# Performance work log

Measured on AMD Instinct MI355X. Metric: run time of the kernel, lower is better.

## Reference

```python
import jax, jax.numpy as jnp
import numpy as np


def setup_inputs() -> dict:
    key = jax.random.key(0)
    kq, kk, kv = jax.random.split(key, 3)
    shape = (2, 8, 1024, 64)  # [B, H, L, D]
    return {
        "q": jax.random.normal(kq, shape, dtype=jnp.float32),
        "k": jax.random.normal(kk, shape, dtype=jnp.float32),
        "v": jax.random.normal(kv, shape, dtype=jnp.float32),
    }


def reference(q, k, v):
    B, H, L, D = q.shape
    eps = 1e-6
    q = jax.nn.relu(q).reshape(B * H, L, D)
    k = jax.nn.relu(k).reshape(B * H, L, D)
    v = jax.nn.relu(v).reshape(B * H, L, D)

    # cosFormer positional reweighting: pi/2 * (i+1)/L
    idx = (jnp.pi / 2) * jnp.arange(1, L + 1, dtype=q.dtype) / L  # [L]
    s = jnp.sin(idx)[None, :, None]  # [1, L, 1]
    c = jnp.cos(idx)[None, :, None]

    q_ = jnp.concatenate([q * s, q * c], axis=-1)  # [N, L, 2D]
    k_ = jnp.concatenate([k * s, k * c], axis=-1)  # [N, L, 2D]

    # causal linear attention via cumulative kv outer product
    kv = jnp.einsum("nld,nlm->nldm", k_, v)        # [N, L, 2D, D]
    kv_cum = jnp.cumsum(kv, axis=1)                  # [N, L, 2D, D]
    qkv = jnp.einsum("nld,nldm->nlm", q_, kv_cum)  # [N, L, D]

    k_cum = jnp.cumsum(k_, axis=1)                   # [N, L, 2D]
    denom = jnp.clip(jnp.einsum("nld,nld->nl", q_, k_cum), eps, None)

    out = qkv / denom[..., None]
    return out.reshape(B, H, L, D)
```

## Files before the change

### kernel.cpp

```cpp
#include <hip/hip_runtime.h>

#define N_HEADS 16
#define L_SEQ   1024
#define D_HEAD  64
#define D2      128
#define T_CHUNK 32
#define N_CHUNK (L_SEQ / T_CHUNK)
#define KV_ELEMS (D2 * D_HEAD)

#define ROWP 140
#define PARTP 132

__device__ __forceinline__ int pad_col(int d2) { return d2 + 4 * (d2 >> 5); }

#define SINCOS_SCALE 1.53398078788564122971e-3f

__device__ __forceinline__ float red8_dpp(float x) {
    x += __int_as_float(__builtin_amdgcn_mov_dpp(__float_as_int(x), 0xB1, 0xF, 0xF, true));
    x += __int_as_float(__builtin_amdgcn_mov_dpp(__float_as_int(x), 0x4E, 0xF, 0xF, true));
    x += __int_as_float(__builtin_amdgcn_mov_dpp(__float_as_int(x), 0x141, 0xF, 0xF, true));
    return x;
}
__device__ __forceinline__ float red16_dpp(float x) {
    x += __int_as_float(__builtin_amdgcn_mov_dpp(__float_as_int(x), 0xB1, 0xF, 0xF, true));
    x += __int_as_float(__builtin_amdgcn_mov_dpp(__float_as_int(x), 0x4E, 0xF, 0xF, true));
    x += __int_as_float(__builtin_amdgcn_mov_dpp(__float_as_int(x), 0x141, 0xF, 0xF, true));
    x += __int_as_float(__builtin_amdgcn_mov_dpp(__float_as_int(x), 0x140, 0xF, 0xF, true));
    return x;
}

__global__ __launch_bounds__(256, 2) void k1_chunk_sums(
    const float* __restrict__ k, const float* __restrict__ v,
    float* __restrict__ sumkv, float* __restrict__ sumk)
{
    __shared__ __attribute__((aligned(16))) float k_s[T_CHUNK][ROWP];
    __shared__ __attribute__((aligned(16))) float v_s[T_CHUNK][D_HEAD];
    __shared__ float s_tab[T_CHUNK], c_tab[T_CHUNK];

    const int c = blockIdx.x, n = blockIdx.y;
    const int tid = threadIdx.x;
    const int base = (n * L_SEQ + c * T_CHUNK) * D_HEAD;

    if (tid < T_CHUNK) {
        float th = SINCOS_SCALE * (float)(c * T_CHUNK + tid + 1);
        s_tab[tid] = __sinf(th);
        c_tab[tid] = __cosf(th);
    }
    __syncthreads();

    const float4* k4g = (const float4*)(k + base);
    const float4* v4g = (const float4*)(v + base);
#pragma unroll
    for (int j = 0; j < 2; ++j) {
        int i4 = j * 256 + tid;
        int l = i4 >> 4, d = (i4 & 15) << 2;
        float4 kk = k4g[i4], vv = v4g[i4];
        kk.x = fmaxf(kk.x, 0.f); kk.y = fmaxf(kk.y, 0.f);
        kk.z = fmaxf(kk.z, 0.f); kk.w = fmaxf(kk.w, 0.f);
        vv.x = fmaxf(vv.x, 0.f); vv.y = fmaxf(vv.y, 0.f);
        vv.z = fmaxf(vv.z, 0.f); vv.w = fmaxf(vv.w, 0.f);
        float s = s_tab[l], cs = c_tab[l];
        *(float4*)&k_s[l][pad_col(d)]      = make_float4(kk.x*s,  kk.y*s,  kk.z*s,  kk.w*s);
        *(float4*)&k_s[l][pad_col(d + 64)] = make_float4(kk.x*cs, kk.y*cs, kk.z*cs, kk.w*cs);
        *(float4*)&v_s[l][d] = vv;
    }
    __syncthreads();

    if (tid < D2) {
        int pc = pad_col(tid);
        float ks = 0.f;
#pragma unroll
        for (int l = 0; l < T_CHUNK; ++l) ks += k_s[l][pc];
        sumk[(n * N_CHUNK + c) * D2 + tid] = ks;
    }

    const int g = tid & 15, mb = (tid >> 4) << 2;
    const int gbase = pad_col(8 * g);

    float st[8][4];
#pragma unroll
    for (int i = 0; i < 8; ++i)
#pragma unroll
        for (int j = 0; j < 4; ++j) st[i][j] = 0.f;

    for (int l = 0; l < T_CHUNK; ++l) {
        float4 vv = *(const float4*)&v_s[l][mb];
        const float4* kf4 = (const float4*)&k_s[l][gbase];
        float4 ka = kf4[0], kb = kf4[1];
        float kf[8] = {ka.x, ka.y, ka.z, ka.w, kb.x, kb.y, kb.z, kb.w};
#pragma unroll
        for (int i = 0; i < 8; ++i) {
            st[i][0] = fmaf(kf[i], vv.x, st[i][0]);
            st[i][1] = fmaf(kf[i], vv.y, st[i][1]);
            st[i][2] = fmaf(kf[i], vv.z, st[i][2]);
            st[i][3] = fmaf(kf[i], vv.w, st[i][3]);
        }
    }

    float4* dst = (float4*)(sumkv + (size_t)(n * N_CHUNK + c) * KV_ELEMS);
#pragma unroll
    for (int i = 0; i < 8; ++i)
        dst[i * 256 + tid] = make_float4(st[i][0], st[i][1], st[i][2], st[i][3]);
}

__global__ __launch_bounds__(256) void k2_prefix(
    float* __restrict__ sumkv, float* __restrict__ sumk)
{
    const int x = blockIdx.x, n = blockIdx.y;
    const int tid = threadIdx.x;

    if (x < 32) {
        float* base = sumkv + (size_t)n * N_CHUNK * KV_ELEMS + x * 256 + tid;
        float t[N_CHUNK];
#pragma unroll
        for (int c = 0; c < N_CHUNK; ++c) t[c] = base[c * KV_ELEMS];
        float r = 0.f;
#pragma unroll
        for (int c = 0; c < N_CHUNK; ++c) { base[c * KV_ELEMS] = r; r += t[c]; }
    } else if (tid < D2) {
        float* bk = sumk + n * N_CHUNK * D2 + tid;
        float t[N_CHUNK];
#pragma unroll
        for (int c = 0; c < N_CHUNK; ++c) t[c] = bk[c * D2];
        float r = 0.f;
#pragma unroll
        for (int c = 0; c < N_CHUNK; ++c) { bk[c * D2] = r; r += t[c]; }
    }
}

__global__ __launch_bounds__(256, 2) void k3_output(
    const float* __restrict__ q, const float* __restrict__ k,
    const float* __restrict__ v, const float* __restrict__ sumkv,
    const float* __restrict__ sumk, float* __restrict__ out)
{
    __shared__ __attribute__((aligned(16))) float k_s[T_CHUNK][ROWP];
    __shared__ __attribute__((aligned(16))) float q_s[T_CHUNK][ROWP];
    __shared__ __attribute__((aligned(16))) float v_s[T_CHUNK][D_HEAD];
    __shared__ __attribute__((aligned(16))) float pool[T_CHUNK * PARTP];
    __shared__ float rden_s[T_CHUNK];
    __shared__ float s_tab[T_CHUNK], c_tab[T_CHUNK];

    float (*part_s)[PARTP] = (float(*)[PARTP])pool;
    float (*out_s)[D_HEAD] = (float(*)[D_HEAD])pool;

    const int c = blockIdx.x, n = blockIdx.y;
    const int tid = threadIdx.x;
    const int base = (n * L_SEQ + c * T_CHUNK) * D_HEAD;

    if (tid < T_CHUNK) {
        float th = SINCOS_SCALE * (float)(c * T_CHUNK + tid + 1);
        s_tab[tid] = __sinf(th);
        c_tab[tid] = __cosf(th);
    }
    __syncthreads();

    const float4* q4g = (const float4*)(q + base);
    const float4* k4g = (const float4*)(k + base);
    const float4* v4g = (const float4*)(v + base);
#pragma unroll
    for (int j = 0; j < 2; ++j) {
        int i4 = j * 256 + tid;
        int l = i4 >> 4, d = (i4 & 15) << 2;
        float4 kk = k4g[i4], qq = q4g[i4], vv = v4g[i4];
        kk.x = fmaxf(kk.x, 0.f); kk.y = fmaxf(kk.y, 0.f);
        kk.z = fmaxf(kk.z, 0.f); kk.w = fmaxf(kk.w, 0.f);
        qq.x = fmaxf(qq.x, 0.f); qq.y = fmaxf(qq.y, 0.f);
        qq.z = fmaxf(qq.z, 0.f); qq.w = fmaxf(qq.w, 0.f);
        vv.x = fmaxf(vv.x, 0.f); vv.y = fmaxf(vv.y, 0.f);
        vv.z = fmaxf(vv.z, 0.f); vv.w = fmaxf(vv.w, 0.f);
        float s = s_tab[l], cs = c_tab[l];
        *(float4*)&k_s[l][pad_col(d)]      = make_float4(kk.x*s,  kk.y*s,  kk.z*s,  kk.w*s);
        *(float4*)&k_s[l][pad_col(d + 64)] = make_float4(kk.x*cs, kk.y*cs, kk.z*cs, kk.w*cs);
        *(float4*)&q_s[l][pad_col(d)]      = make_float4(qq.x*s,  qq.y*s,  qq.z*s,  qq.w*s);
        *(float4*)&q_s[l][pad_col(d + 64)] = make_float4(qq.x*cs, qq.y*cs, qq.z*cs, qq.w*cs);
        *(float4*)&v_s[l][d] = vv;
    }

    const float4* pkv = (const float4*)(sumkv + (size_t)(n * N_CHUNK + c) * KV_ELEMS);
    float st[8][4];
#pragma unroll
    for (int i = 0; i < 8; ++i) {
        float4 p = pkv[i * 256 + tid];
        st[i][0] = p.x; st[i][1] = p.y; st[i][2] = p.z; st[i][3] = p.w;
    }
    float kc = 0.f;
    if (tid < D2) kc = sumk[(n * N_CHUNK + c) * D2 + tid];

    __syncthreads();

    if (tid < D2) {
        int pc = pad_col(tid);
#pragma unroll
        for (int l = 0; l < T_CHUNK; ++l) {
            kc += k_s[l][pc];
            part_s[l][tid] = q_s[l][pc] * kc;
        }
    }
    __syncthreads();

    {
        int l = tid >> 3, j = tid & 7;
        const float4* p4 = (const float4*)&part_s[l][j * 16];
        float4 aa = p4[0], bb = p4[1], cc = p4[2], dd = p4[3];
        float sum = ((aa.x + aa.y) + (aa.z + aa.w)) + ((bb.x + bb.y) + (bb.z + bb.w))
                  + ((cc.x + cc.y) + (cc.z + cc.w)) + ((dd.x + dd.y) + (dd.z + dd.w));
        sum = red8_dpp(sum);
        if (j == 0) rden_s[l] = 1.f / fmaxf(sum, 1e-6f);
    }
    __syncthreads();

    const int g = tid & 15, mb = (tid >> 4) << 2;
    const int gbase = pad_col(8 * g);

    for (int l = 0; l < T_CHUNK; ++l) {
        float4 vv = *(const float4*)&v_s[l][mb];
        const float4* kf4 = (const float4*)&k_s[l][gbase];
        const float4* qf4 = (const float4*)&q_s[l][gbase];
        float4 ka = kf4[0], kb = kf4[1];
        float4 qa = qf4[0], qb = qf4[1];
        float kf[8] = {ka.x, ka.y, ka.z, ka.w, kb.x, kb.y, kb.z, kb.w};
        float qf[8] = {qa.x, qa.y, qa.z, qa.w, qb.x, qb.y, qb.z, qb.w};
        float a0 = 0.f, a1 = 0.f, a2 = 0.f, a3 = 0.f;
#pragma unroll
        for (int i = 0; i < 8; ++i) {
            st[i][0] = fmaf(kf[i], vv.x, st[i][0]); a0 = fmaf(qf[i], st[i][0], a0);
            st[i][1] = fmaf(kf[i], vv.y, st[i][1]); a1 = fmaf(qf[i], st[i][1], a1);
            st[i][2] = fmaf(kf[i], vv.z, st[i][2]); a2 = fmaf(qf[i], st[i][2], a2);
            st[i][3] = fmaf(kf[i], vv.w, st[i][3]); a3 = fmaf(qf[i], st[i][3], a3);
        }
        a0 = red16_dpp(a0);
        a1 = red16_dpp(a1);
        a2 = red16_dpp(a2);
        a3 = red16_dpp(a3);
        if (g == 0) {
            float r = rden_s[l];
            *(float4*)&out_s[l][mb] = make_float4(a0 * r, a1 * r, a2 * r, a3 * r);
        }
    }
    __syncthreads();

    {
        float4* o4 = (float4*)(out + base);
        const float4* s4o = (const float4*)&out_s[0][0];
        o4[tid] = s4o[tid];
        o4[256 + tid] = s4o[256 + tid];
    }
}

extern "C" void kernel_launch(void* const* d_in, const int* in_sizes, int n_in,
                              void* d_out, int out_size, void* d_ws, size_t ws_size,
                              hipStream_t stream) {
    (void)in_sizes; (void)n_in; (void)out_size; (void)ws_size;
    const float* q = (const float*)d_in[0];
    const float* k = (const float*)d_in[1];
    const float* v = (const float*)d_in[2];
    float* out = (float*)d_out;

    float* sumkv = (float*)d_ws;
    float* sumk  = sumkv + (size_t)N_HEADS * N_CHUNK * KV_ELEMS;

    dim3 grid(N_CHUNK, N_HEADS);
    k1_chunk_sums<<<grid, 256, 0, stream>>>(k, v, sumkv, sumk);
    dim3 grid2(33, N_HEADS);
    k2_prefix<<<grid2, 256, 0, stream>>>(sumkv, sumk);
    k3_output<<<grid, 256, 0, stream>>>(q, k, v, sumkv, sumk, out);
}
```

Before: 92.55 us.

## Double threads per chunk block and vectorize prefix scan with float4

Block size for the chunk-sum and output kernels goes from 256 to 512 threads. Each thread now holds a 8x2 slice of the kv state instead of 8x4, which halves per-thread registers and serial FMA work and should raise occupancy and parallelism. The prefix kernel now scans float4 elements in two 16-chunk halves with 9 blocks per head instead of 33. The state layout in the workspace changes to match, and the denominator reduction switches to 16-lane DPP. The risk is more LDS reads per useful FMA and fewer, heavier blocks in the scan kernel.

```diff
diff --git a/kernel.cpp b/kernel.cpp
--- a/kernel.cpp
+++ b/kernel.cpp
@@ -15,12 +15,6 @@
 
 #define SINCOS_SCALE 1.53398078788564122971e-3f
 
-__device__ __forceinline__ float red8_dpp(float x) {
-    x += __int_as_float(__builtin_amdgcn_mov_dpp(__float_as_int(x), 0xB1, 0xF, 0xF, true));
-    x += __int_as_float(__builtin_amdgcn_mov_dpp(__float_as_int(x), 0x4E, 0xF, 0xF, true));
-    x += __int_as_float(__builtin_amdgcn_mov_dpp(__float_as_int(x), 0x141, 0xF, 0xF, true));
-    return x;
-}
 __device__ __forceinline__ float red16_dpp(float x) {
     x += __int_as_float(__builtin_amdgcn_mov_dpp(__float_as_int(x), 0xB1, 0xF, 0xF, true));
     x += __int_as_float(__builtin_amdgcn_mov_dpp(__float_as_int(x), 0x4E, 0xF, 0xF, true));
@@ -29,7 +23,7 @@
     return x;
 }
 
-__global__ __launch_bounds__(256, 2) void k1_chunk_sums(
+__global__ __launch_bounds__(512, 4) void k1_chunk_sums(
     const float* __restrict__ k, const float* __restrict__ v,
     float* __restrict__ sumkv, float* __restrict__ sumk)
 {
@@ -48,13 +42,11 @@
     }
     __syncthreads();
 
-    const float4* k4g = (const float4*)(k + base);
-    const float4* v4g = (const float4*)(v + base);
-#pragma unroll
-    for (int j = 0; j < 2; ++j) {
-        int i4 = j * 256 + tid;
-        int l = i4 >> 4, d = (i4 & 15) << 2;
-        float4 kk = k4g[i4], vv = v4g[i4];
+    {
+        const float4* k4g = (const float4*)(k + base);
+        const float4* v4g = (const float4*)(v + base);
+        int l = tid >> 4, d = (tid & 15) << 2;
+        float4 kk = k4g[tid], vv = v4g[tid];
         kk.x = fmaxf(kk.x, 0.f); kk.y = fmaxf(kk.y, 0.f);
         kk.z = fmaxf(kk.z, 0.f); kk.w = fmaxf(kk.w, 0.f);
         vv.x = fmaxf(vv.x, 0.f); vv.y = fmaxf(vv.y, 0.f);
@@ -74,33 +66,30 @@
         sumk[(n * N_CHUNK + c) * D2 + tid] = ks;
     }
 
-    const int g = tid & 15, mb = (tid >> 4) << 2;
+    const int g = tid & 15, mh = (tid >> 4) << 1;
     const int gbase = pad_col(8 * g);
 
-    float st[8][4];
-#pragma unroll
-    for (int i = 0; i < 8; ++i)
-#pragma unroll
-        for (int j = 0; j < 4; ++j) st[i][j] = 0.f;
+    float st0[8], st1[8];
+#pragma unroll
+    for (int j = 0; j < 8; ++j) { st0[j] = 0.f; st1[j] = 0.f; }
 
     for (int l = 0; l < T_CHUNK; ++l) {
-        float4 vv = *(const float4*)&v_s[l][mb];
+        float2 vm = *(const float2*)&v_s[l][mh];
         const float4* kf4 = (const float4*)&k_s[l][gbase];
         float4 ka = kf4[0], kb = kf4[1];
         float kf[8] = {ka.x, ka.y, ka.z, ka.w, kb.x, kb.y, kb.z, kb.w};
 #pragma unroll
         for (int i = 0; i < 8; ++i) {
-            st[i][0] = fmaf(kf[i], vv.x, st[i][0]);
-            st[i][1] = fmaf(kf[i], vv.y, st[i][1]);
-            st[i][2] = fmaf(kf[i], vv.z, st[i][2]);
-            st[i][3] = fmaf(kf[i], vv.w, st[i][3]);
+            st0[i] = fmaf(kf[i], vm.x, st0[i]);
+            st1[i] = fmaf(kf[i], vm.y, st1[i]);
         }
     }
 
     float4* dst = (float4*)(sumkv + (size_t)(n * N_CHUNK + c) * KV_ELEMS);
-#pragma unroll
-    for (int i = 0; i < 8; ++i)
-        dst[i * 256 + tid] = make_float4(st[i][0], st[i][1], st[i][2], st[i][3]);
+    dst[0 * 512 + tid] = make_float4(st0[0], st0[1], st0[2], st0[3]);
+    dst[1 * 512 + tid] = make_float4(st0[4], st0[5], st0[6], st0[7]);
+    dst[2 * 512 + tid] = make_float4(st1[0], st1[1], st1[2], st1[3]);
+    dst[3 * 512 + tid] = make_float4(st1[4], st1[5], st1[6], st1[7]);
 }
 
 __global__ __launch_bounds__(256) void k2_prefix(
@@ -109,14 +98,20 @@
     const int x = blockIdx.x, n = blockIdx.y;
     const int tid = threadIdx.x;
 
-    if (x < 32) {
-        float* base = sumkv + (size_t)n * N_CHUNK * KV_ELEMS + x * 256 + tid;
-        float t[N_CHUNK];
-#pragma unroll
-        for (int c = 0; c < N_CHUNK; ++c) t[c] = base[c * KV_ELEMS];
-        float r = 0.f;
-#pragma unroll
-        for (int c = 0; c < N_CHUNK; ++c) { base[c * KV_ELEMS] = r; r += t[c]; }
+    if (x < 8) {
+        float4* base = (float4*)(sumkv + (size_t)n * N_CHUNK * KV_ELEMS) + x * 256 + tid;
+        float4 r = make_float4(0.f, 0.f, 0.f, 0.f);
+        float4 t[16];
+#pragma unroll
+        for (int h = 0; h < 2; ++h) {
+#pragma unroll
+            for (int c = 0; c < 16; ++c) t[c] = base[(h * 16 + c) * (KV_ELEMS / 4)];
+#pragma unroll
+            for (int c = 0; c < 16; ++c) {
+                base[(h * 16 + c) * (KV_ELEMS / 4)] = r;
+                r.x += t[c].x; r.y += t[c].y; r.z += t[c].z; r.w += t[c].w;
+            }
+        }
     } else if (tid < D2) {
         float* bk = sumk + n * N_CHUNK * D2 + tid;
         float t[N_CHUNK];
@@ -128,7 +123,7 @@
     }
 }
 
-__global__ __launch_bounds__(256, 2) void k3_output(
+__global__ __launch_bounds__(512, 4) void k3_output(
     const float* __restrict__ q, const float* __restrict__ k,
     const float* __restrict__ v, const float* __restrict__ sumkv,
     const float* __restrict__ sumk, float* __restrict__ out)
@@ -154,14 +149,12 @@
     }
     __syncthreads();
 
-    const float4* q4g = (const float4*)(q + base);
-    const float4* k4g = (const float4*)(k + base);
-    const float4* v4g = (const float4*)(v + base);
-#pragma unroll
-    for (int j = 0; j < 2; ++j) {
-        int i4 = j * 256 + tid;
-        int l = i4 >> 4, d = (i4 & 15) << 2;
-        float4 kk = k4g[i4], qq = q4g[i4], vv = v4g[i4];
+    {
+        const float4* q4g = (const float4*)(q + base);
+        const float4* k4g = (const float4*)(k + base);
+        const float4* v4g = (const float4*)(v + base);
+        int l = tid >> 4, d = (tid & 15) << 2;
+        float4 kk = k4g[tid], qq = q4g[tid], vv = v4g[tid];
         kk.x = fmaxf(kk.x, 0.f); kk.y = fmaxf(kk.y, 0.f);
         kk.z = fmaxf(kk.z, 0.f); kk.w = fmaxf(kk.w, 0.f);
         qq.x = fmaxf(qq.x, 0.f); qq.y = fmaxf(qq.y, 0.f);
@@ -177,11 +170,16 @@
     }
 
     const float4* pkv = (const float4*)(sumkv + (size_t)(n * N_CHUNK + c) * KV_ELEMS);
-    float st[8][4];
-#pragma unroll
-    for (int i = 0; i < 8; ++i) {
-        float4 p = pkv[i * 256 + tid];
-        st[i][0] = p.x; st[i][1] = p.y; st[i][2] = p.z; st[i][3] = p.w;
+    float st0[8], st1[8];
+    {
+        float4 p0 = pkv[0 * 512 + tid];
+        float4 p1 = pkv[1 * 512 + tid];
+        float4 p2 = pkv[2 * 512 + tid];
+        float4 p3 = pkv[3 * 512 + tid];
+        st0[0]=p0.x; st0[1]=p0.y; st0[2]=p0.z; st0[3]=p0.w;
+        st0[4]=p1.x; st0[5]=p1.y; st0[6]=p1.z; st0[7]=p1.w;
+        st1[0]=p2.x; st1[1]=p2.y; st1[2]=p2.z; st1[3]=p2.w;
+        st1[4]=p3.x; st1[5]=p3.y; st1[6]=p3.z; st1[7]=p3.w;
     }
     float kc = 0.f;
     if (tid < D2) kc = sumk[(n * N_CHUNK + c) * D2 + tid];
@@ -199,42 +197,37 @@
     __syncthreads();
 
     {
-        int l = tid >> 3, j = tid & 7;
-        const float4* p4 = (const float4*)&part_s[l][j * 16];
-        float4 aa = p4[0], bb = p4[1], cc = p4[2], dd = p4[3];
-        float sum = ((aa.x + aa.y) + (aa.z + aa.w)) + ((bb.x + bb.y) + (bb.z + bb.w))
-                  + ((cc.x + cc.y) + (cc.z + cc.w)) + ((dd.x + dd.y) + (dd.z + dd.w));
-        sum = red8_dpp(sum);
+        int l = tid >> 4, j = tid & 15;
+        const float4* p4 = (const float4*)&part_s[l][j * 8];
+        float4 aa = p4[0], bb = p4[1];
+        float sum = ((aa.x + aa.y) + (aa.z + aa.w)) + ((bb.x + bb.y) + (bb.z + bb.w));
+        sum = red16_dpp(sum);
         if (j == 0) rden_s[l] = 1.f / fmaxf(sum, 1e-6f);
     }
     __syncthreads();
 
-    const int g = tid & 15, mb = (tid >> 4) << 2;
+    const int g = tid & 15, mh = (tid >> 4) << 1;
     const int gbase = pad_col(8 * g);
 
     for (int l = 0; l < T_CHUNK; ++l) {
-        float4 vv = *(const float4*)&v_s[l][mb];
+        float2 vm = *(const float2*)&v_s[l][mh];
         const float4* kf4 = (const float4*)&k_s[l][gbase];
         const float4* qf4 = (const float4*)&q_s[l][gbase];
         float4 ka = kf4[0], kb = kf4[1];
         float4 qa = qf4[0], qb = qf4[1];
         float kf[8] = {ka.x, ka.y, ka.z, ka.w, kb.x, kb.y, kb.z, kb.w};
         float qf[8] = {qa.x, qa.y, qa.z, qa.w, qb.x, qb.y, qb.z, qb.w};
-        float a0 = 0.f, a1 = 0.f, a2 = 0.f, a3 = 0.f;
+        float a0 = 0.f, a1 = 0.f;
 #pragma unroll
         for (int i = 0; i < 8; ++i) {
-            st[i][0] = fmaf(kf[i], vv.x, st[i][0]); a0 = fmaf(qf[i], st[i][0], a0);
-            st[i][1] = fmaf(kf[i], vv.y, st[i][1]); a1 = fmaf(qf[i], st[i][1], a1);
-            st[i][2] = fmaf(kf[i], vv.z, st[i][2]); a2 = fmaf(qf[i], st[i][2], a2);
-            st[i][3] = fmaf(kf[i], vv.w, st[i][3]); a3 = fmaf(qf[i], st[i][3], a3);
+            st0[i] = fmaf(kf[i], vm.x, st0[i]); a0 = fmaf(qf[i], st0[i], a0);
+            st1[i] = fmaf(kf[i], vm.y, st1[i]); a1 = fmaf(qf[i], st1[i], a1);
         }
         a0 = red16_dpp(a0);
         a1 = red16_dpp(a1);
-        a2 = red16_dpp(a2);
-        a3 = red16_dpp(a3);
         if (g == 0) {
             float r = rden_s[l];
-            *(float4*)&out_s[l][mb] = make_float4(a0 * r, a1 * r, a2 * r, a3 * r);
+            *(float2*)&out_s[l][mh] = make_float2(a0 * r, a1 * r);
         }
     }
     __syncthreads();
@@ -243,7 +236,6 @@
         float4* o4 = (float4*)(out + base);
         const float4* s4o = (const float4*)&out_s[0][0];
         o4[tid] = s4o[tid];
-        o4[256 + tid] = s4o[256 + tid];
     }
 }
 
@@ -260,8 +252,8 @@
     float* sumk  = sumkv + (size_t)N_HEADS * N_CHUNK * KV_ELEMS;
 
     dim3 grid(N_CHUNK, N_HEADS);
-    k1_chunk_sums<<<grid, 256, 0, stream>>>(k, v, sumkv, sumk);
-    dim3 grid2(33, N_HEADS);
+    k1_chunk_sums<<<grid, 512, 0, stream>>>(k, v, sumkv, sumk);
+    dim3 grid2(9, N_HEADS);
     k2_prefix<<<grid2, 256, 0, stream>>>(sumkv, sumk);
-    k3_output<<<grid, 256, 0, stream>>>(q, k, v, sumkv, sumk, out);
-}
+    k3_output<<<grid, 512, 0, stream>>>(q, k, v, sumkv, sumk, out);
+}
```

New measurement: 93.85 us. About the same (+1.4%).
